# Performance work log

Hardware: AMD Instinct MI355X
Metric: run time of the kernel (lower is better)

The kernel has to match this reference:

```python
import jax, jax.numpy as jnp
import numpy as np

N_NODES = 100000


def setup_inputs() -> dict:
    key = jax.random.key(0)
    k1, k2, k3, k4, k5 = jax.random.split(key, 5)
    in_dim, out_dim, n_edges = 128, 128, 640000
    x = jax.random.normal(k1, (N_NODES, in_dim), dtype=jnp.float32)
    src = jax.random.randint(k2, (n_edges,), 0, N_NODES, dtype=jnp.int32)
    dst = jax.random.randint(k3, (n_edges,), 0, N_NODES, dtype=jnp.int32)
    edge_index = jnp.stack([src, dst], axis=0)  # [2, E]
    # nn.Linear default init: U(-1/sqrt(in_dim), 1/sqrt(in_dim))
    bound = 1.0 / np.sqrt(in_dim)
    W = jax.random.uniform(k4, (out_dim, in_dim), minval=-bound, maxval=bound, dtype=jnp.float32)
    b = jax.random.uniform(k5, (out_dim,), minval=-bound, maxval=bound, dtype=jnp.float32)
    return {"x": x, "edge_index": edge_index, "W": W, "b": b}


def reference(x, edge_index, W, b):
    src, dst = edge_index[0], edge_index[1]
    # scatter-sum of gathered source features into destination nodes
    agg = jax.ops.segment_sum(x[src], dst, num_segments=N_NODES)       # [N, d]
    deg = jax.ops.segment_sum(jnp.ones((src.shape[0], 1), x.dtype), dst,
                              num_segments=N_NODES)                     # [N, 1]
    deg = jnp.maximum(deg, 1.0)
    h = agg / deg + x                                                   # mean-agg + residual
    out = jax.nn.relu(h @ W.T + b)                                      # linear + relu (dropout p=0)
    return out
```

## Files before the change

kernel.cpp:

```cpp
#include <hip/hip_runtime.h>
#include <hip/hip_bf16.h>

constexpr int N_NODES = 100000;
constexpr int DIM     = 128;
constexpr int N_EDGES = 640000;

constexpr int CHUNK     = 1024;
constexpr int N_CHUNKS  = (N_NODES + CHUNK - 1) / CHUNK;
constexpr int BINCAP    = 8192;
constexpr int EPB       = 1024;
constexpr int SRC_BITS  = 17;
constexpr int SRC_MASK  = (1 << SRC_BITS) - 1;

constexpr int XCONV_XBLOCKS = N_NODES * DIM / (256 * 8);
constexpr int XCONV_WBLOCKS = DIM * DIM / (256 * 8);

constexpr int HPAD = DIM + 8;

typedef __attribute__((ext_vector_type(4))) float        f32x4;
typedef __attribute__((ext_vector_type(8))) short        bf16x8;
typedef __attribute__((ext_vector_type(4))) unsigned int u32x4;

static __device__ inline unsigned short f2bf(float f) {
    __hip_bfloat16 h = __float2bfloat16(f);
    return *reinterpret_cast<unsigned short*>(&h);
}
static __device__ inline float bf_lo(unsigned u) { return __uint_as_float(u << 16); }
static __device__ inline float bf_hi(unsigned u) { return __uint_as_float(u & 0xffff0000u); }

__global__ __launch_bounds__(256) void gcn_conv(const float* __restrict__ x,
                                                const float* __restrict__ W,
                                                unsigned int* __restrict__ xb,
                                                unsigned int* __restrict__ wb,
                                                int* __restrict__ bincur)
{
    const int b   = blockIdx.x;
    const int gid = b * 256 + threadIdx.x;

    if (b == 0 && threadIdx.x < 128) bincur[threadIdx.x] = 0;

    const float*  src;
    unsigned int* dst;
    int i;
    if (b < XCONV_XBLOCKS) {
        src = x;  dst = xb;  i = gid;
    } else {
        src = W;  dst = wb;  i = gid - XCONV_XBLOCKS * 256;
    }
    const f32x4* s4 = reinterpret_cast<const f32x4*>(src);
    f32x4 a = s4[2 * i];
    f32x4 c = s4[2 * i + 1];
    u32x4 o;
    o.x = (unsigned)f2bf(a.x) | ((unsigned)f2bf(a.y) << 16);
    o.y = (unsigned)f2bf(a.z) | ((unsigned)f2bf(a.w) << 16);
    o.z = (unsigned)f2bf(c.x) | ((unsigned)f2bf(c.y) << 16);
    o.w = (unsigned)f2bf(c.z) | ((unsigned)f2bf(c.w) << 16);
    reinterpret_cast<u32x4*>(dst)[i] = o;
}

__global__ __launch_bounds__(256) void gcn_bin(const int* __restrict__ src,
                                               const int* __restrict__ dst,
                                               int* __restrict__ bincur,
                                               unsigned int* __restrict__ bindata)
{
    __shared__ int bh[N_CHUNKS];
    __shared__ int btb[N_CHUNKS];

    const int t  = threadIdx.x;
    const int e0 = blockIdx.x * EPB + t * 4;

    if (t < N_CHUNKS) bh[t] = 0;
    __syncthreads();

    const int4 s4 = *reinterpret_cast<const int4*>(src + e0);
    const int4 d4 = *reinterpret_cast<const int4*>(dst + e0);

    int bin[4], pos[4];
    unsigned pv[4];
    const int ds[4] = {d4.x, d4.y, d4.z, d4.w};
    const int ss[4] = {s4.x, s4.y, s4.z, s4.w};
    #pragma unroll
    for (int q = 0; q < 4; ++q) {
        bin[q] = ds[q] >> 10;
        pv[q]  = (unsigned)ss[q] | ((unsigned)(ds[q] & (CHUNK - 1)) << SRC_BITS);
        pos[q] = atomicAdd(&bh[bin[q]], 1);
    }
    __syncthreads();

    if (t < N_CHUNKS) btb[t] = atomicAdd(&bincur[t], bh[t]);
    __syncthreads();

    #pragma unroll
    for (int q = 0; q < 4; ++q)
        bindata[(size_t)bin[q] * BINCAP + btb[bin[q]] + pos[q]] = pv[q];
}

__global__ __launch_bounds__(256) void gcn_build(const int* __restrict__ bincur,
                                                 unsigned int* __restrict__ bindata,
                                                 int* __restrict__ off)
{
    __shared__ unsigned stage[BINCAP];
    __shared__ int hist[CHUNK];
    __shared__ int s[256];

    const int c  = blockIdx.x;
    const int t  = threadIdx.x;
    const int nb = min(bincur[c], BINCAP);
    unsigned int* region = bindata + (size_t)c * BINCAP;

    for (int e = t; e < nb; e += 256) stage[e] = region[e];
    #pragma unroll
    for (int q = 0; q < 4; ++q) hist[t + 256 * q] = 0;
    __syncthreads();

    for (int e = t; e < nb; e += 256)
        atomicAdd(&hist[stage[e] >> SRC_BITS], 1);
    __syncthreads();

    int h0 = hist[4 * t + 0], h1 = hist[4 * t + 1];
    int h2 = hist[4 * t + 2], h3 = hist[4 * t + 3];
    s[t] = h0 + h1 + h2 + h3;
    __syncthreads();
    for (int d = 1; d < 256; d <<= 1) {
        int add = (t >= d) ? s[t - d] : 0;
        __syncthreads();
        s[t] += add;
        __syncthreads();
    }
    int excl = (t > 0) ? s[t - 1] : 0;

    const int st0 = excl;
    const int st1 = excl + h0;
    const int st2 = excl + h0 + h1;
    const int st3 = excl + h0 + h1 + h2;
    hist[4 * t + 0] = st0;  hist[4 * t + 1] = st1;
    hist[4 * t + 2] = st2;  hist[4 * t + 3] = st3;

    const int nbase = c * CHUNK;
    if (nbase + 4 * t + 0 < N_NODES) off[nbase + 4 * t + 0] = st0 | (h0 << 13);
    if (nbase + 4 * t + 1 < N_NODES) off[nbase + 4 * t + 1] = st1 | (h1 << 13);
    if (nbase + 4 * t + 2 < N_NODES) off[nbase + 4 * t + 2] = st2 | (h2 << 13);
    if (nbase + 4 * t + 3 < N_NODES) off[nbase + 4 * t + 3] = st3 | (h3 << 13);
    __syncthreads();

    for (int e = t; e < nb; e += 256) {
        unsigned v  = stage[e];
        int slot    = atomicAdd(&hist[v >> SRC_BITS], 1);
        region[slot] = v & SRC_MASK;
    }
}

static __device__ inline void acc8(float* acc, u32x4 v) {
    #pragma unroll
    for (int q = 0; q < 4; ++q) {
        unsigned u = v[q];
        acc[2 * q]     += bf_lo(u);
        acc[2 * q + 1] += bf_hi(u);
    }
}

__global__ __launch_bounds__(256) void gcn_gmm(
    const unsigned short* __restrict__ xb,
    const int* __restrict__ off,
    const unsigned int* __restrict__ csr,
    const unsigned short* __restrict__ wb,
    const float* __restrict__ bias,
    float* __restrict__ out)
{
    __shared__ unsigned short hl[16][HPAD];

    const int tid    = threadIdx.x;
    const int n0     = blockIdx.x * 16;
    const int nloc   = tid >> 4;
    const int lane16 = tid & 15;
    const int col8   = lane16 * 8;
    const int n      = n0 + nloc;

    {
        const int meta  = off[n];
        const int count = meta >> 13;
        const int start = (n >> 10) * BINCAP + (meta & (BINCAP - 1));
        const int end   = start + count;

        float acc[8];
        #pragma unroll
        for (int q = 0; q < 8; ++q) acc[q] = 0.0f;

        int i = start;
        for (; i + 4 <= end; i += 4) {
            int s0 = csr[i], s1 = csr[i + 1], s2 = csr[i + 2], s3 = csr[i + 3];
            u32x4 v0 = *reinterpret_cast<const u32x4*>(xb + (size_t)s0 * DIM + col8);
            u32x4 v1 = *reinterpret_cast<const u32x4*>(xb + (size_t)s1 * DIM + col8);
            u32x4 v2 = *reinterpret_cast<const u32x4*>(xb + (size_t)s2 * DIM + col8);
            u32x4 v3 = *reinterpret_cast<const u32x4*>(xb + (size_t)s3 * DIM + col8);
            acc8(acc, v0); acc8(acc, v1); acc8(acc, v2); acc8(acc, v3);
        }
        for (; i < end; ++i) {
            u32x4 v = *reinterpret_cast<const u32x4*>(xb + (size_t)csr[i] * DIM + col8);
            acc8(acc, v);
        }

        const float inv = 1.0f / fmaxf((float)count, 1.0f);
        const u32x4 xr = *reinterpret_cast<const u32x4*>(xb + (size_t)n * DIM + col8);
        u32x4 o;
        #pragma unroll
        for (int q = 0; q < 4; ++q) {
            float v0 = acc[2 * q]     * inv + bf_lo(xr[q]);
            float v1 = acc[2 * q + 1] * inv + bf_hi(xr[q]);
            o[q] = (unsigned)f2bf(v0) | ((unsigned)f2bf(v1) << 16);
        }
        *reinterpret_cast<u32x4*>(&hl[nloc][col8]) = o;
    }
    __syncthreads();

    const int w    = tid >> 6;
    const int lane = tid & 63;
    const int r    = lane & 15;
    const int g    = lane >> 4;

    bf16x8 af[4];
    #pragma unroll
    for (int t = 0; t < 4; ++t)
        af[t] = *reinterpret_cast<const bf16x8*>(&hl[r][32 * t + 8 * g]);

    #pragma unroll
    for (int cc = 0; cc < 2; ++cc) {
        const int c = 2 * w + cc;
        f32x4 acc = {0.f, 0.f, 0.f, 0.f};
        #pragma unroll
        for (int t = 0; t < 4; ++t) {
            bf16x8 wf = *reinterpret_cast<const bf16x8*>(
                wb + (16 * c + r) * DIM + 32 * t + 8 * g);
            acc = __builtin_amdgcn_mfma_f32_16x16x32_bf16(af[t], wf, acc, 0, 0, 0);
        }
        const float bj = bias[16 * c + r];
        #pragma unroll
        for (int q = 0; q < 4; ++q)
            out[(size_t)(n0 + 4 * g + q) * DIM + 16 * c + r] =
                fmaxf(acc[q] + bj, 0.0f);
    }
}

extern "C" void kernel_launch(void* const* d_in, const int* in_sizes, int n_in,
                              void* d_out, int out_size, void* d_ws, size_t ws_size,
                              hipStream_t stream)
{
    const float* x    = (const float*)d_in[0];
    const int*   eidx = (const int*)d_in[1];
    const float* W    = (const float*)d_in[2];
    const float* bias = (const float*)d_in[3];
    float*       out  = (float*)d_out;

    const int* src = eidx;
    const int* dst = eidx + N_EDGES;

    int* bincur = (int*)d_ws;
    int* off    = bincur + 128;
    unsigned int* bindata = (unsigned int*)(off + 100352);
    unsigned short* wb = (unsigned short*)(bindata + (size_t)N_CHUNKS * BINCAP);
    unsigned short* xb = wb + (size_t)DIM * DIM;

    gcn_conv <<<XCONV_XBLOCKS + XCONV_WBLOCKS, 256, 0, stream>>>(
        x, W, (unsigned int*)xb, (unsigned int*)wb, bincur);
    gcn_bin  <<<N_EDGES / EPB, 256, 0, stream>>>(src, dst, bincur, bindata);
    gcn_build<<<N_CHUNKS, 256, 0, stream>>>(bincur, bindata, off);
    gcn_gmm  <<<N_NODES / 16, 256, 0, stream>>>(
        xb, off, bindata, wb, bias, out);
}
```

Measured before the change: 96.74 us.

## Apply linear transform before aggregation and fuse conversion into GEMM

Uses linearity to compute y = x·Wᵀ first, in a GEMM kernel that converts x and W to bf16 on the fly and stores y as bf16. The aggregation kernel then gathers rows of y, takes their mean, adds the residual y row, bias and relu, and writes the output. This removes the separate conversion pass and the MFMA stage that followed aggregation. The gather volume stays the same. Each GEMM block reloads and converts the full W into shared memory. Rounding y to bf16 changes where precision is lost relative to the reference.

```diff
diff --git a/kernel.cpp b/kernel.cpp
--- a/kernel.cpp
+++ b/kernel.cpp
@@ -12,10 +12,7 @@
 constexpr int SRC_BITS  = 17;
 constexpr int SRC_MASK  = (1 << SRC_BITS) - 1;
 
-constexpr int XCONV_XBLOCKS = N_NODES * DIM / (256 * 8);
-constexpr int XCONV_WBLOCKS = DIM * DIM / (256 * 8);
-
-constexpr int HPAD = DIM + 8;
+constexpr int YNB = 32;
 
 typedef __attribute__((ext_vector_type(4))) float        f32x4;
 typedef __attribute__((ext_vector_type(8))) short        bf16x8;
@@ -28,34 +25,69 @@
 static __device__ inline float bf_lo(unsigned u) { return __uint_as_float(u << 16); }
 static __device__ inline float bf_hi(unsigned u) { return __uint_as_float(u & 0xffff0000u); }
 
-__global__ __launch_bounds__(256) void gcn_conv(const float* __restrict__ x,
-                                                const float* __restrict__ W,
-                                                unsigned int* __restrict__ xb,
-                                                unsigned int* __restrict__ wb,
-                                                int* __restrict__ bincur)
-{
-    const int b   = blockIdx.x;
-    const int gid = b * 256 + threadIdx.x;
-
-    if (b == 0 && threadIdx.x < 128) bincur[threadIdx.x] = 0;
-
-    const float*  src;
-    unsigned int* dst;
-    int i;
-    if (b < XCONV_XBLOCKS) {
-        src = x;  dst = xb;  i = gid;
-    } else {
-        src = W;  dst = wb;  i = gid - XCONV_XBLOCKS * 256;
-    }
-    const f32x4* s4 = reinterpret_cast<const f32x4*>(src);
-    f32x4 a = s4[2 * i];
-    f32x4 c = s4[2 * i + 1];
-    u32x4 o;
-    o.x = (unsigned)f2bf(a.x) | ((unsigned)f2bf(a.y) << 16);
-    o.y = (unsigned)f2bf(a.z) | ((unsigned)f2bf(a.w) << 16);
-    o.z = (unsigned)f2bf(c.x) | ((unsigned)f2bf(c.y) << 16);
-    o.w = (unsigned)f2bf(c.z) | ((unsigned)f2bf(c.w) << 16);
-    reinterpret_cast<u32x4*>(dst)[i] = o;
+static __device__ inline bf16x8 pack8(f32x4 a, f32x4 b) {
+    bf16x8 v;
+    v[0] = (short)f2bf(a.x); v[1] = (short)f2bf(a.y);
+    v[2] = (short)f2bf(a.z); v[3] = (short)f2bf(a.w);
+    v[4] = (short)f2bf(b.x); v[5] = (short)f2bf(b.y);
+    v[6] = (short)f2bf(b.z); v[7] = (short)f2bf(b.w);
+    return v;
+}
+
+__global__ __launch_bounds__(256) void gcn_gemm_y(
+    const float* __restrict__ x,
+    const float* __restrict__ W,
+    unsigned short* __restrict__ y,
+    int* __restrict__ bincur)
+{
+    __shared__ unsigned short wl[DIM][DIM + 8];
+
+    const int tid = threadIdx.x;
+    const int n0  = blockIdx.x * YNB;
+
+    if (blockIdx.x == 0 && tid < 128) bincur[tid] = 0;
+
+    #pragma unroll
+    for (int rep = 0; rep < 8; ++rep) {
+        const int e   = rep * 2048 + tid * 8;
+        const int row = e >> 7;
+        const int col = e & 127;
+        f32x4 a = *reinterpret_cast<const f32x4*>(W + e);
+        f32x4 b = *reinterpret_cast<const f32x4*>(W + e + 4);
+        *reinterpret_cast<bf16x8*>(&wl[row][col]) = pack8(a, b);
+    }
+    __syncthreads();
+
+    const int w    = tid >> 6;
+    const int lane = tid & 63;
+    const int r    = lane & 15;
+    const int g    = lane >> 4;
+    const int rowt  = w & 1;
+    const int cbase = 4 * (w >> 1);
+
+    bf16x8 af[4];
+    #pragma unroll
+    for (int t = 0; t < 4; ++t) {
+        const float* xp = x + (size_t)(n0 + 16 * rowt + r) * DIM + 32 * t + 8 * g;
+        f32x4 a = *reinterpret_cast<const f32x4*>(xp);
+        f32x4 b = *reinterpret_cast<const f32x4*>(xp + 4);
+        af[t] = pack8(a, b);
+    }
+
+    #pragma unroll
+    for (int cc = 0; cc < 4; ++cc) {
+        const int c = cbase + cc;
+        f32x4 acc = {0.f, 0.f, 0.f, 0.f};
+        #pragma unroll
+        for (int t = 0; t < 4; ++t) {
+            bf16x8 wf = *reinterpret_cast<const bf16x8*>(&wl[16 * c + r][32 * t + 8 * g]);
+            acc = __builtin_amdgcn_mfma_f32_16x16x32_bf16(af[t], wf, acc, 0, 0, 0);
+        }
+        #pragma unroll
+        for (int q = 0; q < 4; ++q)
+            y[(size_t)(n0 + 16 * rowt + 4 * g + q) * DIM + 16 * c + r] =
+                f2bf(acc[q]);
+    }
 }
 
 __global__ __launch_bounds__(256) void gcn_bin(const int* __restrict__ src,
@@ -159,86 +191,57 @@
     }
 }
 
-__global__ __launch_bounds__(256) void gcn_gmm(
-    const unsigned short* __restrict__ xb,
+__global__ __launch_bounds__(256) void gcn_agg(
+    const unsigned short* __restrict__ y,
     const int* __restrict__ off,
     const unsigned int* __restrict__ csr,
-    const unsigned short* __restrict__ wb,
     const float* __restrict__ bias,
     float* __restrict__ out)
 {
-    __shared__ unsigned short hl[16][HPAD];
-
     const int tid    = threadIdx.x;
-    const int n0     = blockIdx.x * 16;
-    const int nloc   = tid >> 4;
     const int lane16 = tid & 15;
+    const int n      = blockIdx.x * 16 + (tid >> 4);
     const int col8   = lane16 * 8;
-    const int n      = n0 + nloc;
-
-    {
-        const int meta  = off[n];
-        const int count = meta >> 13;
-        const int start = (n >> 10) * BINCAP + (meta & (BINCAP - 1));
-        const int end   = start + count;
-
-        float acc[8];
-        #pragma unroll
-        for (int q = 0; q < 8; ++q) acc[q] = 0.0f;
-
-        int i = start;
-        for (; i + 4 <= end; i += 4) {
-            int s0 = csr[i], s1 = csr[i + 1], s2 = csr[i + 2], s3 = csr[i + 3];
-            u32x4 v0 = *reinterpret_cast<const u32x4*>(xb + (size_t)s0 * DIM + col8);
-            u32x4 v1 = *reinterpret_cast<const u32x4*>(xb + (size_t)s1 * DIM + col8);
-            u32x4 v2 = *reinterpret_cast<const u32x4*>(xb + (size_t)s2 * DIM + col8);
-            u32x4 v3 = *reinterpret_cast<const u32x4*>(xb + (size_t)s3 * DIM + col8);
-            acc8(acc, v0); acc8(acc, v1); acc8(acc, v2); acc8(acc, v3);
-        }
-        for (; i < end; ++i) {
-            u32x4 v = *reinterpret_cast<const u32x4*>(xb + (size_t)csr[i] * DIM + col8);
-            acc8(acc, v);
-        }
-
-        const float inv = 1.0f / fmaxf((float)count, 1.0f);
-        const u32x4 xr = *reinterpret_cast<const u32x4*>(xb + (size_t)n * DIM + col8);
-        u32x4 o;
-        #pragma unroll
-        for (int q = 0; q < 4; ++q) {
-            float v0 = acc[2 * q]     * inv + bf_lo(xr[q]);
-            float v1 = acc[2 * q + 1] * inv + bf_hi(xr[q]);
-            o[q] = (unsigned)f2bf(v0) | ((unsigned)f2bf(v1) << 16);
-        }
-        *reinterpret_cast<u32x4*>(&hl[nloc][col8]) = o;
-    }
-    __syncthreads();
-
-    const int w    = tid >> 6;
-    const int lane = tid & 63;
-    const int r    = lane & 15;
-    const int g    = lane >> 4;
-
-    bf16x8 af[4];
-    #pragma unroll
-    for (int t = 0; t < 4; ++t)
-        af[t] = *reinterpret_cast<const bf16x8*>(&hl[r][32 * t + 8 * g]);
-
-    #pragma unroll
-    for (int cc = 0; cc < 2; ++cc) {
-        const int c = 2 * w + cc;
-        f32x4 acc = {0.f, 0.f, 0.f, 0.f};
-        #pragma unroll
-        for (int t = 0; t < 4; ++t) {
-            bf16x8 wf = *reinterpret_cast<const bf16x8*>(
-                wb + (16 * c + r) * DIM + 32 * t + 8 * g);
-            acc = __builtin_amdgcn_mfma_f32_16x16x32_bf16(af[t], wf, acc, 0, 0, 0);
-        }
-        const float bj = bias[16 * c + r];
-        #pragma unroll
-        for (int q = 0; q < 4; ++q)
-            out[(size_t)(n0 + 4 * g + q) * DIM + 16 * c + r] =
-                fmaxf(acc[q] + bj, 0.0f);
-    }
+
+    const int meta  = off[n];
+    const int count = meta >> 13;
+    int i           = (n >> 10) * BINCAP + (meta & (BINCAP - 1));
+    const int end   = i + count;
+
+    float acc[8];
+    #pragma unroll
+    for (int q = 0; q < 8; ++q) acc[q] = 0.0f;
+
+    for (; i + 4 <= end; i += 4) {
+        int s0 = csr[i], s1 = csr[i + 1], s2 = csr[i + 2], s3 = csr[i + 3];
+        u32x4 v0 = *reinterpret_cast<const u32x4*>(y + (size_t)s0 * DIM + col8);
+        u32x4 v1 = *reinterpret_cast<const u32x4*>(y + (size_t)s1 * DIM + col8);
+        u32x4 v2 = *reinterpret_cast<const u32x4*>(y + (size_t)s2 * DIM + col8);
+        u32x4 v3 = *reinterpret_cast<const u32x4*>(y + (size_t)s3 * DIM + col8);
+        acc8(acc, v0); acc8(acc, v1); acc8(acc, v2); acc8(acc, v3);
+    }
+    for (; i < end; ++i) {
+        u32x4 v = *reinterpret_cast<const u32x4*>(y + (size_t)csr[i] * DIM + col8);
+        acc8(acc, v);
+    }
+
+    const float inv = 1.0f / fmaxf((float)count, 1.0f);
+    const u32x4 yr = *reinterpret_cast<const u32x4*>(y + (size_t)n * DIM + col8);
+    const f32x4 b0 = *reinterpret_cast<const f32x4*>(bias + col8);
+    const f32x4 b1 = *reinterpret_cast<const f32x4*>(bias + col8 + 4);
+
+    f32x4 o0, o1;
+    o0.x = fmaxf(acc[0] * inv + bf_lo(yr[0]) + b0.x, 0.0f);
+    o0.y = fmaxf(acc[1] * inv + bf_hi(yr[0]) + b0.y, 0.0f);
+    o0.z = fmaxf(acc[2] * inv + bf_lo(yr[1]) + b0.z, 0.0f);
+    o0.w = fmaxf(acc[3] * inv + bf_hi(yr[1]) + b0.w, 0.0f);
+    o1.x = fmaxf(acc[4] * inv + bf_lo(yr[2]) + b1.x, 0.0f);
+    o1.y = fmaxf(acc[5] * inv + bf_hi(yr[2]) + b1.y, 0.0f);
+    o1.z = fmaxf(acc[6] * inv + bf_lo(yr[3]) + b1.z, 0.0f);
+    o1.w = fmaxf(acc[7] * inv + bf_hi(yr[3]) + b1.w, 0.0f);
+
+    *reinterpret_cast<f32x4*>(out + (size_t)n * DIM + col8)     = o0;
+    *reinterpret_cast<f32x4*>(out + (size_t)n * DIM + col8 + 4) = o1;
 }
 
 extern "C" void kernel_launch(void* const* d_in, const int* in_sizes, int n_in,
@@ -257,13 +260,10 @@
     int* bincur = (int*)d_ws;
     int* off    = bincur + 128;
     unsigned int* bindata = (unsigned int*)(off + 100352);
-    unsigned short* wb = (unsigned short*)(bindata + (size_t)N_CHUNKS * BINCAP);
-    unsigned short* xb = wb + (size_t)DIM * DIM;
-
-    gcn_conv <<<XCONV_XBLOCKS + XCONV_WBLOCKS, 256, 0, stream>>>(
-        x, W, (unsigned int*)xb, (unsigned int*)wb, bincur);
-    gcn_bin  <<<N_EDGES / EPB, 256, 0, stream>>>(src, dst, bincur, bindata);
-    gcn_build<<<N_CHUNKS, 256, 0, stream>>>(bincur, bindata, off);
-    gcn_gmm  <<<N_NODES / 16, 256, 0, stream>>>(
-        xb, off, bindata, wb, bias, out);
-}
+    unsigned short* y = (unsigned short*)(bindata + (size_t)N_CHUNKS * BINCAP);
+
+    gcn_gemm_y<<<N_NODES / YNB, 256, 0, stream>>>(x, W, y, bincur);
+    gcn_bin   <<<N_EDGES / EPB, 256, 0, stream>>>(src, dst, bincur, bindata);
+    gcn_build <<<N_CHUNKS, 256, 0, stream>>>(bincur, bindata, off);
+    gcn_agg   <<<N_NODES / 16, 256, 0, stream>>>(y, off, bindata, bias, out);
+}
```

After: 90.85 us, median of 2. 1.06x faster.
